# Kernel optimization log

Measured on AMD Instinct MI355X. Metric: run time of the kernel, lower is better.

Reference implementation:

```python
import jax, jax.numpy as jnp
import numpy as np

B, T, C_IN, H, W = 8, 12, 64, 64, 64
HID = 128
K = 3
NUM_CLASSES = 5


def _conv2d(x, w, b):
    # x: (B, Cin, H, W), w: (Cout, Cin, k, k) -> (B, Cout, H, W), SAME padding
    y = jax.lax.conv_general_dilated(
        x, w, window_strides=(1, 1), padding='SAME',
        dimension_numbers=('NCHW', 'OIHW', 'NCHW'))
    return y + b[None, :, None, None]


def setup_inputs() -> dict:
    key = jax.random.key(0)
    ks = jax.random.split(key, 5)
    inputs = jax.random.normal(ks[0], (B, T, C_IN, H, W), dtype=jnp.float32)
    # ConvLSTM gate conv: concat(x, h) channels -> 4*hidden gate channels
    fan_in = (C_IN + HID) * K * K
    w_lstm = jax.random.normal(ks[1], (4 * HID, C_IN + HID, K, K), dtype=jnp.float32) / np.sqrt(fan_in)
    b_lstm = jnp.zeros((4 * HID,), dtype=jnp.float32)
    w_conv = jax.random.normal(ks[2], (NUM_CLASSES, HID, K, K), dtype=jnp.float32) / np.sqrt(HID * K * K)
    b_conv = jnp.zeros((NUM_CLASSES,), dtype=jnp.float32)
    return {'inputs': inputs, 'w_lstm': w_lstm, 'b_lstm': b_lstm,
            'w_conv': w_conv, 'b_conv': b_conv}


def _clstm(inputs, w_lstm, b_lstm):
    # inputs: (B, T, C, H, W); returns final hidden state (B, HID, H, W)
    xs = jnp.transpose(inputs, (1, 0, 2, 3, 4))  # (T, B, C, H, W)
    h0 = jnp.zeros((inputs.shape[0], HID, H, W), dtype=inputs.dtype)
    c0 = jnp.zeros_like(h0)

    def step(carry, x_t):
        h, c = carry
        combined = jnp.concatenate([x_t, h], axis=1)           # (B, C+HID, H, W)
        gates = _conv2d(combined, w_lstm, b_lstm)              # (B, 4*HID, H, W)
        cc_i, cc_f, cc_o, cc_g = jnp.split(gates, 4, axis=1)
        i = jax.nn.sigmoid(cc_i)
        f = jax.nn.sigmoid(cc_f)
        o = jax.nn.sigmoid(cc_o)
        g = jnp.tanh(cc_g)
        c_next = f * c + i * g
        h_next = o * jnp.tanh(c_next)
        return (h_next, c_next), None

    (h_T, _), _ = jax.lax.scan(step, (h0, c0), xs)
    return h_T


def reference(inputs, w_lstm, b_lstm, w_conv, b_conv):
    final_state = _clstm(inputs, w_lstm, b_lstm)               # (B, HID, H, W)
    scores = _conv2d(final_state, w_conv, b_conv)              # (B, NUM_CLASSES, H, W)
    # Softmax2d over channels followed by log == channelwise log_softmax
    preds = jax.nn.log_softmax(scores, axis=1)
    return preds
```

## Files before the change

kernel.cpp:

```cpp
#include <hip/hip_runtime.h>
#include <math.h>

#define BB   8
#define TT   12

typedef _Float16 f16;
typedef f16  f16x8 __attribute__((ext_vector_type(8)));
typedef float f32x4 __attribute__((ext_vector_type(4)));

#define OFF_WT2  0ull
#define OFF_WC   1818624ull
#define OFF_XP   1855488ull
#define OFF_HA   6451200ull
#define OFF_HB   15642624ull
#define OFF_C    24834048ull
#define WS_END   41611264ull
#define ZERO_BYTES (WS_END - OFF_XP)

#define A_BYTES 52800
#define B_BYTES 37888

__device__ inline void gload16(const void* g, void* l) {
    __builtin_amdgcn_global_load_lds((const __attribute__((address_space(1))) void*)g,
                                     (__attribute__((address_space(3))) void*)l, 16, 0, 0);
}

__device__ inline float sigm_fast(float x) {
    return 1.f / (1.f + __expf(-x));
}
__device__ inline float tanh_fast(float x) {
    float xx = fminf(fmaxf(x, -15.f), 15.f);
    float e = __expf(2.f * xx);
    return (e - 1.f) / (e + 1.f);
}

__global__ __launch_bounds__(256) void zero_kernel(float4* __restrict__ p, int n4) {
    int i = blockIdx.x * blockDim.x + threadIdx.x;
    int stride = gridDim.x * blockDim.x;
    for (; i < n4; i += stride) p[i] = make_float4(0.f, 0.f, 0.f, 0.f);
}

__global__ __launch_bounds__(256) void wprep(const float* __restrict__ w, f16* __restrict__ wT2) {
    int t = blockIdx.x * 256 + threadIdx.x;
    if (t >= 8 * 6 * 64 * 296) return;
    int k    = t % 296;
    int r    = t / 296;
    int co_l = r & 63;
    int r2   = r >> 6;
    int chunk = r2 % 6;
    int ntl   = r2 / 6;
    f16 val = (f16)0.f;
    if (k < 288) {
        int tap = k >> 5, ci_l = k & 31;
        int ci  = chunk * 32 + ci_l;
        int cop = ntl * 64 + co_l;
        int hid = cop >> 2, gate = cop & 3;
        val = (f16)w[((size_t)(gate * 128 + hid) * 192 + ci) * 9 + tap];
    }
    wT2[t] = val;
}

__global__ __launch_bounds__(256) void wcprep(const float* __restrict__ w, float* __restrict__ wc) {
    int t = blockIdx.x * 256 + threadIdx.x;
    if (t >= 9216) return;
    int cls = t & 7, ci = (t >> 3) & 127, tap = t >> 10;
    wc[t] = (cls < 5) ? w[(size_t)(cls * 128 + ci) * 9 + tap] : 0.f;
}

__global__ __launch_bounds__(256) void xprep(const float* __restrict__ x, f16* __restrict__ xp, int t) {
    int pos = blockIdx.x * 256 + threadIdx.x;
    int b = pos >> 12, rr = pos & 4095, y = rr >> 6, xx = rr & 63;
    const float* s = x + ((size_t)(b * TT + t) * 64) * 4096 + y * 64 + xx;
    f16* d = xp + (((size_t)b * 66 + y + 1) * 68 + xx + 1) * 64;
    #pragma unroll
    for (int c8 = 0; c8 < 8; ++c8) {
        f16x8 v;
        #pragma unroll
        for (int e = 0; e < 8; ++e) v[e] = (f16)s[(size_t)(c8 * 8 + e) * 4096];
        *(f16x8*)&d[c8 * 8] = v;
    }
}

__device__ inline float pickc(f32x4 v, int j) {
    return j == 0 ? v[0] : j == 1 ? v[1] : j == 2 ? v[2] : v[3];
}

__global__ __launch_bounds__(512, 2) void gemm_step(
    const f16* __restrict__ xp, const f16* __restrict__ hin,
    const f16* __restrict__ wT2, const float* __restrict__ b_lstm,
    float* __restrict__ c_st, f16* __restrict__ hout)
{
    __shared__ __align__(16) char smem[A_BYTES + 2 * B_BYTES];
    f16* As  = (f16*)smem;
    char* Bs0 = smem + A_BYTES;
    char* Bs1 = smem + A_BYTES + B_BYTES;

    const int tid  = threadIdx.x;
    const int lane = tid & 63;
    const int wid  = tid >> 6;
    const int l15  = lane & 15, lg = lane >> 4;

    const int bid = blockIdx.x;
    const int nt  = bid >> 6;
    const int mt  = bid & 63;
    const int b   = mt >> 3;
    const int yr  = (mt & 7) << 3;

    const int rowbase = (b * 66 + yr) * 68;
    const f16* wslice = wT2 + (size_t)(nt * 6) * 18944;

    f32x4 acc[4][4] = {};
    f16x8 areg[6];

    int po[6], wo[6], c8o[6];
    bool av[6];
    #pragma unroll
    for (int i = 0; i < 6; ++i) {
        int idx = i * 512 + tid;
        av[i] = idx < 2640;
        int ci8 = idx & 3;
        int pc  = idx >> 2;
        int r   = (pc * 497) >> 15;
        int c   = pc - r * 66;
        po[i]  = rowbase + r * 68 + c;
        c8o[i] = ci8 * 8;
        wo[i]  = pc * 40 + ci8 * 8;
    }

    auto loadA = [&](int cc) {
        if (cc < 2) {
            const f16* src = xp + cc * 32;
            #pragma unroll
            for (int i = 0; i < 6; ++i)
                if (av[i]) areg[i] = *(const f16x8*)(src + ((size_t)po[i] << 6) + c8o[i]);
        } else {
            const f16* src = hin + (cc * 32 - 64);
            #pragma unroll
            for (int i = 0; i < 6; ++i)
                if (av[i]) areg[i] = *(const f16x8*)(src + ((size_t)po[i] << 7) + c8o[i]);
        }
    };
    auto writeA = [&]() {
        #pragma unroll
        for (int i = 0; i < 6; ++i)
            if (av[i]) *(f16x8*)&As[wo[i]] = areg[i];
    };
    auto stageB = [&](int cc, char* Bs) {
        const char* bsrc = (const char*)(wslice + (size_t)cc * 18944);
        for (int k = wid; k < 37; k += 8)
            gload16(bsrc + k * 1024 + lane * 16, Bs + k * 1024);
    };
    auto compute = [&](const f16* Bsf) {
        #pragma unroll
        for (int tap = 0; tap < 9; ++tap) {
            const int dy = tap / 3, dx = tap - dy * 3;
            f16x8 a[4];
            #pragma unroll
            for (int mf = 0; mf < 4; ++mf)
                a[mf] = *(const f16x8*)&As[((wid + dy) * 66 + mf * 16 + l15 + dx) * 40 + lg * 8];
            f16x8 bf[4];
            #pragma unroll
            for (int nf = 0; nf < 4; ++nf)
                bf[nf] = *(const f16x8*)&Bsf[(nf * 16 + l15) * 296 + tap * 32 + lg * 8];
            #pragma unroll
            for (int mf = 0; mf < 4; ++mf)
                #pragma unroll
                for (int nf = 0; nf < 4; ++nf)
                    acc[mf][nf] = __builtin_amdgcn_mfma_f32_16x16x32_f16(a[mf], bf[nf], acc[mf][nf], 0, 0, 0);
        }
    };

    loadA(0);
    stageB(0, Bs0);
    writeA();
    __syncthreads();

    char* Bcur = Bs0; char* Balt = Bs1;

    #pragma unroll 1
    for (int cc = 0; cc < 6; ++cc) {
        if (cc < 5) {
            stageB(cc + 1, Balt);
            loadA(cc + 1);
        }
        compute((const f16*)Bcur);
        if (cc < 5) {
            __syncthreads();
            writeA();
            __syncthreads();
            char* tb = Bcur; Bcur = Balt; Balt = tb;
        }
    }

    const int q = lane & 3;
    #pragma unroll
    for (int mf = 0; mf < 4; ++mf) {
        #pragma unroll
        for (int nf = 0; nf < 4; ++nf) {
            int hid = nt * 16 + nf * 4 + (l15 >> 2);
            float bias = b_lstm[q * 128 + hid];
            f32x4 v = acc[mf][nf];
            v[0] += bias; v[1] += bias; v[2] += bias; v[3] += bias;
            float own = pickc(v, q);
            float r1 = __shfl_xor(pickc(v, q ^ 1), 1);
            float r2 = __shfl_xor(pickc(v, q ^ 2), 2);
            float r3 = __shfl_xor(pickc(v, q ^ 3), 3);
            float gi = q == 0 ? own : (q == 1 ? r1 : q == 2 ? r2 : r3);
            float gf = q == 1 ? own : (q == 0 ? r1 : q == 3 ? r2 : r3);
            float go = q == 2 ? own : (q == 3 ? r1 : q == 0 ? r2 : r3);
            float gg = q == 3 ? own : (q == 2 ? r1 : q == 1 ? r2 : r3);
            float i_ = sigm_fast(gi);
            float f_ = sigm_fast(gf);
            float o_ = sigm_fast(go);
            float g_ = tanh_fast(gg);
            int px = mf * 16 + lg * 4 + q;
            int py = yr + wid;
            size_t ic = (((size_t)b * 64 + py) * 64 + px) * 128 + hid;
            float cv = f_ * c_st[ic] + i_ * g_;
            c_st[ic] = cv;
            float hv = o_ * tanh_fast(cv);
            hout[(((size_t)b * 66 + py + 1) * 68 + (px + 1)) * 128 + hid] = (f16)hv;
        }
    }
}

__global__ __launch_bounds__(256) void final_conv(
    const f16* __restrict__ h, const float* __restrict__ wc,
    const float* __restrict__ b_conv, float* __restrict__ out)
{
    __shared__ float swc[9216];
    for (int i = threadIdx.x; i < 9216; i += 256) swc[i] = wc[i];
    __syncthreads();
    int pos = blockIdx.x * 256 + threadIdx.x;
    int b = pos >> 12, rr = pos & 4095, y = rr >> 6, xx = rr & 63;
    float acc[5];
    #pragma unroll
    for (int cls = 0; cls < 5; ++cls) acc[cls] = b_conv[cls];
    #pragma unroll 1
    for (int tap = 0; tap < 9; ++tap) {
        int dy = tap / 3, dx = tap - dy * 3;
        const f16* hp = h + (((size_t)b * 66 + y + dy) * 68 + xx + dx) * 128;
        #pragma unroll
        for (int c16 = 0; c16 < 16; ++c16) {
            f16x8 v = *(const f16x8*)&hp[c16 * 8];
            #pragma unroll
            for (int e = 0; e < 8; ++e) {
                float hv = (float)v[e];
                const float* wp = &swc[(size_t)(tap * 128 + c16 * 8 + e) * 8];
                acc[0] = fmaf(hv, wp[0], acc[0]);
                acc[1] = fmaf(hv, wp[1], acc[1]);
                acc[2] = fmaf(hv, wp[2], acc[2]);
                acc[3] = fmaf(hv, wp[3], acc[3]);
                acc[4] = fmaf(hv, wp[4], acc[4]);
            }
        }
    }
    float m = acc[0];
    #pragma unroll
    for (int cls = 1; cls < 5; ++cls) m = fmaxf(m, acc[cls]);
    float s = 0.f;
    #pragma unroll
    for (int cls = 0; cls < 5; ++cls) s += __expf(acc[cls] - m);
    float lse = logf(s) + m;
    #pragma unroll
    for (int cls = 0; cls < 5; ++cls)
        out[((size_t)(b * 5 + cls) << 12) + (y << 6) + xx] = acc[cls] - lse;
}

extern "C" void kernel_launch(void* const* d_in, const int* in_sizes, int n_in,
                              void* d_out, int out_size, void* d_ws, size_t ws_size,
                              hipStream_t stream) {
    const float* x      = (const float*)d_in[0];
    const float* w_lstm = (const float*)d_in[1];
    const float* b_lstm = (const float*)d_in[2];
    const float* w_conv = (const float*)d_in[3];
    const float* b_conv = (const float*)d_in[4];
    char* ws = (char*)d_ws;
    f16*   wT2 = (f16*)(ws + OFF_WT2);
    float* wc  = (float*)(ws + OFF_WC);
    f16*   xp  = (f16*)(ws + OFF_XP);
    f16*   hA  = (f16*)(ws + OFF_HA);
    f16*   hB  = (f16*)(ws + OFF_HB);
    float* c   = (float*)(ws + OFF_C);

    zero_kernel<<<2048, 256, 0, stream>>>((float4*)(ws + OFF_XP), (int)(ZERO_BYTES / 16));
    wprep<<<3552, 256, 0, stream>>>(w_lstm, wT2);
    wcprep<<<36, 256, 0, stream>>>(w_conv, wc);

    for (int t = 0; t < TT; ++t) {
        const f16* hin  = (t & 1) ? hB : hA;
        f16*       hout = (t & 1) ? hA : hB;
        xprep<<<128, 256, 0, stream>>>(x, xp, t);
        gemm_step<<<512, 512, 0, stream>>>(xp, hin, wT2, b_lstm, c, hout);
    }
    final_conv<<<128, 256, 0, stream>>>(hA, wc, b_conv, (float*)d_out);
}
```

Before: 986.4 us.

## Double-buffer A tile via direct global-to-LDS loads with XOR swizzle, 256-thread blocks

The activation tile now goes straight from global memory into LDS using buffer-to-LDS loads, replacing the register staging and the extra barrier. A is double-buffered like B, leaving one sync per channel chunk. The A layout changes from a padded 40-halfs row stride to a dense 32-halfs stride with an XOR swizzle to limit bank conflicts. Blocks shrink to 256 threads, with each wave computing two output rows (8x4 MFMA accumulators). This doubles the register load per wave and raises LDS use to about 160KB per block, which lowers occupancy to one block per CU.

Result: slower. 1.037 ms (+5.1%).

```diff
diff --git a/kernel.cpp b/kernel.cpp
--- a/kernel.cpp
+++ b/kernel.cpp
@@ -17,7 +17,7 @@
 #define WS_END   41611264ull
 #define ZERO_BYTES (WS_END - OFF_XP)
 
-#define A_BYTES 52800
+#define A_BYTES 43008
 #define B_BYTES 37888
 
 __device__ inline void gload16(const void* g, void* l) {
@@ -85,15 +85,16 @@
     return j == 0 ? v[0] : j == 1 ? v[1] : j == 2 ? v[2] : v[3];
 }
 
-__global__ __launch_bounds__(512, 2) void gemm_step(
+__global__ __launch_bounds__(256, 1) void gemm_step(
     const f16* __restrict__ xp, const f16* __restrict__ hin,
     const f16* __restrict__ wT2, const float* __restrict__ b_lstm,
     float* __restrict__ c_st, f16* __restrict__ hout)
 {
-    __shared__ __align__(16) char smem[A_BYTES + 2 * B_BYTES];
-    f16* As  = (f16*)smem;
-    char* Bs0 = smem + A_BYTES;
-    char* Bs1 = smem + A_BYTES + B_BYTES;
+    __shared__ __align__(16) char smem[2 * A_BYTES + 2 * B_BYTES];
+    char* Ab0 = smem;
+    char* Ab1 = smem + A_BYTES;
+    char* Bb0 = smem + 2 * A_BYTES;
+    char* Bb1 = smem + 2 * A_BYTES + B_BYTES;
 
     const int tid  = threadIdx.x;
     const int lane = tid & 63;
@@ -109,112 +110,107 @@
     const int rowbase = (b * 66 + yr) * 68;
     const f16* wslice = wT2 + (size_t)(nt * 6) * 18944;
 
-    f32x4 acc[4][4] = {};
-    f16x8 areg[6];
-
-    int po[6], wo[6], c8o[6];
-    bool av[6];
-    #pragma unroll
-    for (int i = 0; i < 6; ++i) {
-        int idx = i * 512 + tid;
-        av[i] = idx < 2640;
-        int ci8 = idx & 3;
-        int pc  = idx >> 2;
-        int r   = (pc * 497) >> 15;
-        int c   = pc - r * 66;
-        po[i]  = rowbase + r * 68 + c;
-        c8o[i] = ci8 * 8;
-        wo[i]  = pc * 40 + ci8 * 8;
-    }
-
-    auto loadA = [&](int cc) {
-        if (cc < 2) {
-            const f16* src = xp + cc * 32;
-            #pragma unroll
-            for (int i = 0; i < 6; ++i)
-                if (av[i]) areg[i] = *(const f16x8*)(src + ((size_t)po[i] << 6) + c8o[i]);
-        } else {
-            const f16* src = hin + (cc * 32 - 64);
-            #pragma unroll
-            for (int i = 0; i < 6; ++i)
-                if (av[i]) areg[i] = *(const f16x8*)(src + ((size_t)po[i] << 7) + c8o[i]);
+    f32x4 acc[8][4] = {};
+
+    int poA[11], cxA[11];
+    #pragma unroll
+    for (int i = 0; i < 11; ++i) {
+        int k = wid + i * 4;
+        int item = k * 64 + lane;
+        int pc = item >> 2;
+        int s  = item & 3;
+        int pcc = pc < 660 ? pc : 0;
+        int r = (pcc * 497) >> 15;
+        int c = pcc - r * 66;
+        poA[i] = rowbase + r * 68 + c;
+        cxA[i] = (s ^ ((pcc >> 1) & 3)) * 8;
+    }
+
+    auto stageA = [&](int cc, char* Ad) {
+        const f16* act; int sh, ci0;
+        if (cc < 2) { act = xp;  sh = 6; ci0 = cc * 32; }
+        else        { act = hin; sh = 7; ci0 = cc * 32 - 64; }
+        #pragma unroll
+        for (int i = 0; i < 11; ++i) {
+            int k = wid + i * 4;
+            if (k < 42)
+                gload16(act + (((size_t)poA[i]) << sh) + ci0 + cxA[i], Ad + k * 1024);
         }
     };
-    auto writeA = [&]() {
-        #pragma unroll
-        for (int i = 0; i < 6; ++i)
-            if (av[i]) *(f16x8*)&As[wo[i]] = areg[i];
+    auto stageB = [&](int cc, char* Bd) {
+        const char* bsrc = (const char*)(wslice + (size_t)cc * 18944);
+        for (int k = wid; k < 37; k += 4)
+            gload16(bsrc + k * 1024 + lane * 16, Bd + k * 1024);
     };
-    auto stageB = [&](int cc, char* Bs) {
-        const char* bsrc = (const char*)(wslice + (size_t)cc * 18944);
-        for (int k = wid; k < 37; k += 8)
-            gload16(bsrc + k * 1024 + lane * 16, Bs + k * 1024);
-    };
-    auto compute = [&](const f16* Bsf) {
+    auto compute = [&](const char* Abuf, const char* Bbuf) {
+        const f16* As  = (const f16*)Abuf;
+        const f16* Bsf = (const f16*)Bbuf;
         #pragma unroll
         for (int tap = 0; tap < 9; ++tap) {
             const int dy = tap / 3, dx = tap - dy * 3;
-            f16x8 a[4];
-            #pragma unroll
-            for (int mf = 0; mf < 4; ++mf)
-                a[mf] = *(const f16x8*)&As[((wid + dy) * 66 + mf * 16 + l15 + dx) * 40 + lg * 8];
+            f16x8 a[8];
+            #pragma unroll
+            for (int r2 = 0; r2 < 2; ++r2)
+                #pragma unroll
+                for (int mf = 0; mf < 4; ++mf) {
+                    int p = (wid * 2 + r2 + dy) * 66 + mf * 16 + l15 + dx;
+                    a[r2 * 4 + mf] = *(const f16x8*)&As[p * 32 + ((lg ^ ((p >> 1) & 3)) << 3)];
+                }
             f16x8 bf[4];
             #pragma unroll
             for (int nf = 0; nf < 4; ++nf)
                 bf[nf] = *(const f16x8*)&Bsf[(nf * 16 + l15) * 296 + tap * 32 + lg * 8];
             #pragma unroll
-            for (int mf = 0; mf < 4; ++mf)
+            for (int m = 0; m < 8; ++m)
                 #pragma unroll
                 for (int nf = 0; nf < 4; ++nf)
-                    acc[mf][nf] = __builtin_amdgcn_mfma_f32_16x16x32_f16(a[mf], bf[nf], acc[mf][nf], 0, 0, 0);
+                    acc[m][nf] = __builtin_amdgcn_mfma_f32_16x16x32_f16(a[m], bf[nf], acc[m][nf], 0, 0, 0);
         }
     };
 
-    loadA(0);
-    stageB(0, Bs0);
-    writeA();
+    stageA(0, Ab0);
+    stageB(0, Bb0);
     __syncthreads();
 
-    char* Bcur = Bs0; char* Balt = Bs1;
+    char* Ac = Ab0; char* Aa = Ab1;
+    char* Bc = Bb0; char* Ba = Bb1;
 
     #pragma unroll 1
     for (int cc = 0; cc < 6; ++cc) {
         if (cc < 5) {
-            stageB(cc + 1, Balt);
-            loadA(cc + 1);
-        }
-        compute((const f16*)Bcur);
-        if (cc < 5) {
-            __syncthreads();
-            writeA();
-            __syncthreads();
-            char* tb = Bcur; Bcur = Balt; Balt = tb;
-        }
+            stageA(cc + 1, Aa);
+            stageB(cc + 1, Ba);
+        }
+        compute(Ac, Bc);
+        __syncthreads();
+        char* t1 = Ac; Ac = Aa; Aa = t1;
+        char* t2 = Bc; Bc = Ba; Ba = t2;
     }
 
     const int q = lane & 3;
     #pragma unroll
-    for (int mf = 0; mf < 4; ++mf) {
+    for (int m = 0; m < 8; ++m) {
+        const int r2 = m >> 2, mf = m & 3;
         #pragma unroll
         for (int nf = 0; nf < 4; ++nf) {
             int hid = nt * 16 + nf * 4 + (l15 >> 2);
             float bias = b_lstm[q * 128 + hid];
-            f32x4 v = acc[mf][nf];
+            f32x4 v = acc[m][nf];
             v[0] += bias; v[1] += bias; v[2] += bias; v[3] += bias;
             float own = pickc(v, q);
             float r1 = __shfl_xor(pickc(v, q ^ 1), 1);
-            float r2 = __shfl_xor(pickc(v, q ^ 2), 2);
+            float rr2 = __shfl_xor(pickc(v, q ^ 2), 2);
             float r3 = __shfl_xor(pickc(v, q ^ 3), 3);
-            float gi = q == 0 ? own : (q == 1 ? r1 : q == 2 ? r2 : r3);
-            float gf = q == 1 ? own : (q == 0 ? r1 : q == 3 ? r2 : r3);
-            float go = q == 2 ? own : (q == 3 ? r1 : q == 0 ? r2 : r3);
-            float gg = q == 3 ? own : (q == 2 ? r1 : q == 1 ? r2 : r3);
+            float gi = q == 0 ? own : (q == 1 ? r1 : q == 2 ? rr2 : r3);
+            float gf = q == 1 ? own : (q == 0 ? r1 : q == 3 ? rr2 : r3);
+            float go = q == 2 ? own : (q == 3 ? r1 : q == 0 ? rr2 : r3);
+            float gg = q == 3 ? own : (q == 2 ? r1 : q == 1 ? rr2 : r3);
             float i_ = sigm_fast(gi);
             float f_ = sigm_fast(gf);
             float o_ = sigm_fast(go);
             float g_ = tanh_fast(gg);
             int px = mf * 16 + lg * 4 + q;
-            int py = yr + wid;
+            int py = yr + wid * 2 + r2;
             size_t ic = (((size_t)b * 64 + py) * 64 + px) * 128 + hid;
             float cv = f_ * c_st[ic] + i_ * g_;
             c_st[ic] = cv;
@@ -291,7 +287,7 @@
         const f16* hin  = (t & 1) ? hB : hA;
         f16*       hout = (t & 1) ? hA : hB;
         xprep<<<128, 256, 0, stream>>>(x, xp, t);
-        gemm_step<<<512, 512, 0, stream>>>(xp, hin, wT2, b_lstm, c, hout);
+        gemm_step<<<512, 256, 0, stream>>>(xp, hin, wT2, b_lstm, c, hout);
     }
     final_conv<<<128, 256, 0, stream>>>(hA, wc, b_conv, (float*)d_out);
 }
```
